# Performance work log

Measured on AMD Instinct MI355X. Metric: run time of the kernel, lower is better.

Reference implementation:

```python
import jax, jax.numpy as jnp
import numpy as np

D = 1024
BATCH = 32768
QJL_DIM = 1024

# Optimal 3-bit (8-level) Lloyd-Max quantizer for the standard normal N(0,1).
# Rotated coordinates of Gaussian inputs are ~N(0,1) since Pi is orthogonal.
_CENTROIDS = np.array([-2.1520, -1.3439, -0.7560, -0.2451,
                        0.2451,  0.7560,  1.3439,  2.1520], dtype=np.float32)
_BOUNDARIES = np.array([-1.7480, -1.0500, -0.5006, 0.0,
                         0.5006,  1.0500,  1.7480], dtype=np.float32)


def setup_inputs() -> dict:
    key = jax.random.key(0)
    kx, kpi, ks = jax.random.split(key, 3)
    x = jax.random.normal(kx, (BATCH, D), dtype=jnp.float32)
    # Haar rotation: orthogonal matrix via QR of a Gaussian matrix
    G = jax.random.normal(kpi, (D, D), dtype=jnp.float32)
    Pi, _ = jnp.linalg.qr(G)
    # QJL projection matrix: iid N(0,1), shape (m, d)
    S = jax.random.normal(ks, (QJL_DIM, D), dtype=jnp.float32)
    return {
        "x": x,
        "Pi": Pi,
        "S": S,
        "centroids": jnp.asarray(_CENTROIDS),
        "boundaries": jnp.asarray(_BOUNDARIES),
    }


def reference(x, Pi, S, centroids, boundaries):
    # --- Stage 1: MSE quantizer (rotate -> Lloyd-Max -> unrotate) ---
    y = x @ Pi.T                                  # (B, d) rotated coordinates
    idx = jnp.searchsorted(boundaries, y)         # (B, d) int32 in [0, 8)
    y_hat = centroids[idx]                        # (B, d) per-coordinate dequant
    x_hat = y_hat @ Pi                            # unrotate back to original frame

    # --- Stage 2: QJL on the residual ---
    residual = x - x_hat                          # (B, d)
    residual_norm = jnp.linalg.norm(residual, axis=-1)   # (B,)
    projected = residual @ S.T                    # (B, m)
    # torch.sign with sign(0) forced to +1
    qjl_signs = jnp.where(projected >= 0, 1.0, -1.0).astype(x.dtype)

    return (idx, qjl_signs, residual_norm)
```

## Files before the change

### kernel.cpp

```cpp
#include <hip/hip_runtime.h>

#define DK 1024
#define NB 32768
#define BM 128
#define BN 128
#define BKT 32
#define NKT (DK / BKT)
#define FLUSH_KT 15

typedef const __attribute__((address_space(1))) void GAS;
typedef __attribute__((address_space(3))) void LAS;

__device__ __forceinline__ void gll16(const void* g, void* l) {
    __builtin_amdgcn_global_load_lds((GAS*)g, (LAS*)l, 16, 0, 0);
}

template<int MODE>
__global__ __launch_bounds__(256)
void gk(const float* __restrict__ A,
        const float* __restrict__ W,
        const float* __restrict__ X,
        const float* __restrict__ cent,
        const float* __restrict__ bnd,
        float* __restrict__ out)
{
    __shared__ float As[2][BM * BKT];
    __shared__ float Bs[2][BN * BKT];
    __shared__ float centS[8];

    const int tid  = threadIdx.x;
    const int lane = tid & 63;
    const int wid  = tid >> 6;
    const int tx8 = tid & 15, ty8 = tid >> 4;
    const int m0 = blockIdx.y * BM;
    const int n0 = blockIdx.x * BN;

    const int lr = lane >> 3;
    const int gs = lane & 7;

    const int arow = tid >> 1;
    const int ah   = (tid & 1) * 4;
    const int akey = (arow >> 3) & 7;
    float4 pidx[4];

    if (MODE == 1 && tid < 8) centS[tid] = cent[tid];

    auto stageNT = [&](float* dst, const float* src, int rowbase, int kt) {
#pragma unroll
        for (int q = 0; q < 4; ++q) {
            const int rb  = wid * 32 + q * 8;
            const int key = (rb >> 3) & 7;
            const float* gp = src + (size_t)(rowbase + rb + lr) * DK
                                  + kt * BKT + ((gs ^ key) << 2);
            gll16(gp, dst + rb * BKT);
        }
    };
    auto stageNN = [&](float* dst, const float* src, int kt) {
#pragma unroll
        for (int q = 0; q < 4; ++q) {
            const int r2 = (wid * 4 + q) * 2;
            const float* gp = src + (size_t)(kt * BKT + r2 + (lane >> 5)) * DK
                                  + n0 + ((lane & 31) << 2);
            gll16(gp, dst + r2 * BN);
        }
    };
    auto loadIdx = [&](int kt) {
#pragma unroll
        for (int g = 0; g < 4; ++g)
            pidx[g] = *(const float4*)&A[(size_t)(m0 + arow) * DK + kt * BKT + (ah + g) * 4];
    };
    auto writeA = [&](float* dst) {
#pragma unroll
        for (int g = 0; g < 4; ++g) {
            float4 v;
            v.x = centS[(int)pidx[g].x];
            v.y = centS[(int)pidx[g].y];
            v.z = centS[(int)pidx[g].z];
            v.w = centS[(int)pidx[g].w];
            *(float4*)&dst[arow * BKT + (((ah + g) ^ akey) << 2)] = v;
        }
    };

    float chn[8][8];
#pragma unroll
    for (int i = 0; i < 8; ++i)
#pragma unroll
        for (int j = 0; j < 8; ++j) chn[i][j] = 0.0f;

    const int akr = ty8 & 7;
    const int bkr = tx8 & 7;

    if (MODE == 1) { loadIdx(0); stageNN(Bs[0], W, 0); }
    else           { stageNT(As[0], A, m0, 0); stageNT(Bs[0], W, n0, 0); }
    __syncthreads();
    if (MODE == 1) { writeA(As[0]); __syncthreads(); }

    int cur = 0;
    for (int kt = 0; kt < NKT; ++kt) {
        if (kt + 1 < NKT) {
            if (MODE == 1) { loadIdx(kt + 1); stageNN(Bs[cur ^ 1], W, kt + 1); }
            else { stageNT(As[cur ^ 1], A, m0, kt + 1);
                   stageNT(Bs[cur ^ 1], W, n0, kt + 1); }
        }

        const float4* As4 = (const float4*)As[cur];
        const float4* Bs4 = (const float4*)Bs[cur];
#pragma unroll
        for (int c = 0; c < 8; ++c) {
            float4 a4[8];
#pragma unroll
            for (int i = 0; i < 8; ++i)
                a4[i] = As4[(ty8 * 8 + i) * 8 + (c ^ akr)];
            if constexpr (MODE != 1) {
                float4 b4[8];
#pragma unroll
                for (int j = 0; j < 8; ++j)
                    b4[j] = Bs4[(tx8 * 8 + j) * 8 + (c ^ bkr)];
#pragma unroll
                for (int e = 0; e < 4; ++e)
#pragma unroll
                    for (int i = 0; i < 8; ++i)
#pragma unroll
                        for (int j = 0; j < 8; ++j)
                            chn[i][j] = fmaf(((const float*)&a4[i])[e],
                                             ((const float*)&b4[j])[e], chn[i][j]);
            } else {
#pragma unroll
                for (int e = 0; e < 4; ++e) {
                    const float4 b0 = *(const float4*)&Bs[cur][(c * 4 + e) * BN + tx8 * 8];
                    const float4 b1 = *(const float4*)&Bs[cur][(c * 4 + e) * BN + tx8 * 8 + 4];
                    const float b[8] = {b0.x, b0.y, b0.z, b0.w, b1.x, b1.y, b1.z, b1.w};
#pragma unroll
                    for (int i = 0; i < 8; ++i)
#pragma unroll
                        for (int j = 0; j < 8; ++j)
                            chn[i][j] = fmaf(((const float*)&a4[i])[e], b[j], chn[i][j]);
                }
            }
        }

        if (kt == FLUSH_KT) {
#pragma unroll
            for (int i = 0; i < 8; ++i) {
                const int row = m0 + ty8 * 8 + i;
#pragma unroll
                for (int jq = 0; jq < 2; ++jq) {
                    float4 v;
                    v.x = chn[i][jq * 4 + 0];
                    v.y = chn[i][jq * 4 + 1];
                    v.z = chn[i][jq * 4 + 2];
                    v.w = chn[i][jq * 4 + 3];
                    *(float4*)&out[(size_t)row * DK + n0 + tx8 * 8 + jq * 4] = v;
                    chn[i][jq * 4 + 0] = 0.0f;
                    chn[i][jq * 4 + 1] = 0.0f;
                    chn[i][jq * 4 + 2] = 0.0f;
                    chn[i][jq * 4 + 3] = 0.0f;
                }
            }
        }

        if (MODE == 1 && kt + 1 < NKT) writeA(As[cur ^ 1]);
        __syncthreads();
        cur ^= 1;
    }

    if constexpr (MODE == 0) {
        float bb[7];
#pragma unroll
        for (int t = 0; t < 7; ++t) bb[t] = bnd[t];
#pragma unroll
        for (int i = 0; i < 8; ++i) {
            const int row = m0 + ty8 * 8 + i;
#pragma unroll
            for (int jq = 0; jq < 2; ++jq) {
                const int col = n0 + tx8 * 8 + jq * 4;
                const float4 p = *(const float4*)&out[(size_t)row * DK + col];
                float4 v;
#pragma unroll
                for (int e = 0; e < 4; ++e) {
                    const float yf = ((const float*)&p)[e] + chn[i][jq * 4 + e];
                    int id = 0;
#pragma unroll
                    for (int t = 0; t < 7; ++t) id += (yf > bb[t]) ? 1 : 0;
                    ((float*)&v)[e] = (float)id;
                }
                *(float4*)&out[(size_t)row * DK + col] = v;
            }
        }
    } else if constexpr (MODE == 1) {
#pragma unroll
        for (int i = 0; i < 8; ++i) {
            const int row = m0 + ty8 * 8 + i;
#pragma unroll
            for (int jq = 0; jq < 2; ++jq) {
                const int col = n0 + tx8 * 8 + jq * 4;
                const float4 p  = *(const float4*)&out[(size_t)row * DK + col];
                const float4 xv = *(const float4*)&X[(size_t)row * DK + col];
                float4 v;
                v.x = xv.x - (p.x + chn[i][jq * 4 + 0]);
                v.y = xv.y - (p.y + chn[i][jq * 4 + 1]);
                v.z = xv.z - (p.z + chn[i][jq * 4 + 2]);
                v.w = xv.w - (p.w + chn[i][jq * 4 + 3]);
                *(float4*)&out[(size_t)row * DK + col] = v;
            }
        }
    } else {
#pragma unroll
        for (int i = 0; i < 8; ++i) {
            const int row = m0 + ty8 * 8 + i;
#pragma unroll
            for (int jq = 0; jq < 2; ++jq) {
                const int col = n0 + tx8 * 8 + jq * 4;
                const float4 p = *(const float4*)&out[(size_t)row * DK + col];
                float4 v;
#pragma unroll
                for (int e = 0; e < 4; ++e)
                    ((float*)&v)[e] =
                        ((((const float*)&p)[e] + chn[i][jq * 4 + e]) >= 0.0f)
                            ? 1.0f : -1.0f;
                *(float4*)&out[(size_t)row * DK + col] = v;
            }
        }
    }
}

__global__ __launch_bounds__(256)
void norm_k(const float* __restrict__ resid, float* __restrict__ outn)
{
    const int lane = threadIdx.x & 63;
    const int row  = blockIdx.x * 4 + (threadIdx.x >> 6);
    const float* r = &resid[(size_t)row * DK];
    double s = 0.0;
    for (int i = lane; i < DK; i += 64) {
        const double v = (double)r[i];
        s += v * v;
    }
#pragma unroll
    for (int off = 32; off > 0; off >>= 1)
        s += __shfl_xor(s, off, 64);
    if (lane == 0) outn[row] = (float)sqrt(s);
}

__global__ __launch_bounds__(256)
void stage2_band(const float* __restrict__ RS,
                 const float* __restrict__ Sm,
                 float* __restrict__ out_sign,
                 float* __restrict__ out_norm)
{
    __shared__ float Rs[16][DK + 1];
    __shared__ float Bsh[16][64];

    const int tid = threadIdx.x;
    const int m0  = blockIdx.x * 16;

    for (int c = tid; c < 16 * 256; c += 256) {
        const int row = c >> 8, q = c & 255;
        const float4 v = *(const float4*)&RS[(size_t)(m0 + row) * DK + q * 4];
        Rs[row][q * 4 + 0] = v.x;
        Rs[row][q * 4 + 1] = v.y;
        Rs[row][q * 4 + 2] = v.z;
        Rs[row][q * 4 + 3] = v.w;
    }
    __syncthreads();

    {
        const int row = tid >> 4, sub = tid & 15;
        double s = 0.0;
        for (int c = sub; c < DK; c += 16) {
            const double v = (double)Rs[row][c];
            s += v * v;
        }
        s += __shfl_xor(s, 1, 16);
        s += __shfl_xor(s, 2, 16);
        s += __shfl_xor(s, 4, 16);
        s += __shfl_xor(s, 8, 16);
        if (sub == 0) out_norm[m0 + row] = (float)sqrt(s);
    }

    const int tx = tid & 15, ty = tid >> 4;
    const int srow = tid >> 2, s4 = tid & 3;

    for (int nt = 0; nt < 16; ++nt) {
        const int n0 = nt * 64;
        float chn[4] = {0.f, 0.f, 0.f, 0.f}, tot[4] = {0.f, 0.f, 0.f, 0.f};

        for (int kt = 0; kt < 64; ++kt) {
            const int k0 = kt * 16;
            __syncthreads();
            const float4 w = *(const float4*)&Sm[(size_t)(n0 + srow) * DK + k0 + s4 * 4];
            Bsh[s4 * 4 + 0][srow] = w.x;
            Bsh[s4 * 4 + 1][srow] = w.y;
            Bsh[s4 * 4 + 2][srow] = w.z;
            Bsh[s4 * 4 + 3][srow] = w.w;
            __syncthreads();
#pragma unroll
            for (int kk = 0; kk < 16; ++kk) {
                const float a = Rs[ty][k0 + kk];
#pragma unroll
                for (int j = 0; j < 4; ++j)
                    chn[j] = fmaf(a, Bsh[kk][tx * 4 + j], chn[j]);
            }
            if (kt == 31) {
#pragma unroll
                for (int j = 0; j < 4; ++j) { tot[j] += chn[j]; chn[j] = 0.0f; }
            }
        }
#pragma unroll
        for (int j = 0; j < 4; ++j) tot[j] += chn[j];
#pragma unroll
        for (int j = 0; j < 4; ++j)
            out_sign[(size_t)(m0 + ty) * DK + n0 + tx * 4 + j] =
                (tot[j] >= 0.0f) ? 1.0f : -1.0f;
    }
}

extern "C" void kernel_launch(void* const* d_in, const int* in_sizes, int n_in,
                              void* d_out, int out_size, void* d_ws, size_t ws_size,
                              hipStream_t stream)
{
    const float* x    = (const float*)d_in[0];
    const float* Pi   = (const float*)d_in[1];
    const float* S    = (const float*)d_in[2];
    const float* cent = (const float*)d_in[3];
    const float* bnd  = (const float*)d_in[4];

    float* out_idx  = (float*)d_out;
    float* out_sign = out_idx + (size_t)NB * DK;
    float* out_norm = out_idx + 2 * (size_t)NB * DK;

    const dim3 grid(DK / BN, NB / BM);
    const size_t needF32 = (size_t)NB * DK * sizeof(float);

    gk<0><<<grid, 256, 0, stream>>>(x, Pi, (const float*)nullptr, cent, bnd, out_idx);

    if (ws_size >= needF32) {
        float* resid = (float*)d_ws;
        gk<1><<<grid, 256, 0, stream>>>(out_idx, Pi, x, cent, bnd, resid);
        gk<2><<<grid, 256, 0, stream>>>(resid, S, (const float*)nullptr, cent, bnd, out_sign);
        norm_k<<<NB / 4, 256, 0, stream>>>(resid, out_norm);
    } else {
        gk<1><<<grid, 256, 0, stream>>>(out_idx, Pi, x, cent, bnd, out_sign);
        stage2_band<<<NB / 16, 256, 0, stream>>>(out_sign, S, out_sign, out_norm);
    }
}
```

Measured before the change: 3.383 ms.

## Read A operand directly from global and emit dequantized y_hat from stage one

After: 3.292 ms. 1.03x faster.

```diff
diff --git a/kernel.cpp b/kernel.cpp
--- a/kernel.cpp
+++ b/kernel.cpp
@@ -22,9 +22,9 @@
         const float* __restrict__ X,
         const float* __restrict__ cent,
         const float* __restrict__ bnd,
-        float* __restrict__ out)
+        float* __restrict__ out,
+        float* __restrict__ yout)
 {
-    __shared__ float As[2][BM * BKT];
     __shared__ float Bs[2][BN * BKT];
     __shared__ float centS[8];
 
@@ -38,19 +38,14 @@
     const int lr = lane >> 3;
     const int gs = lane & 7;
 
-    const int arow = tid >> 1;
-    const int ah   = (tid & 1) * 4;
-    const int akey = (arow >> 3) & 7;
-    float4 pidx[4];
-
-    if (MODE == 1 && tid < 8) centS[tid] = cent[tid];
-
-    auto stageNT = [&](float* dst, const float* src, int rowbase, int kt) {
+    if (MODE == 0 && tid < 8) centS[tid] = cent[tid];
+
+    auto stageNT = [&](float* dst, const float* src, int kt) {
 #pragma unroll
         for (int q = 0; q < 4; ++q) {
             const int rb  = wid * 32 + q * 8;
             const int key = (rb >> 3) & 7;
-            const float* gp = src + (size_t)(rowbase + rb + lr) * DK
+            const float* gp = src + (size_t)(n0 + rb + lr) * DK
                                   + kt * BKT + ((gs ^ key) << 2);
             gll16(gp, dst + rb * BKT);
         }
@@ -64,22 +59,9 @@
             gll16(gp, dst + r2 * BN);
         }
     };
-    auto loadIdx = [&](int kt) {
-#pragma unroll
-        for (int g = 0; g < 4; ++g)
-            pidx[g] = *(const float4*)&A[(size_t)(m0 + arow) * DK + kt * BKT + (ah + g) * 4];
-    };
-    auto writeA = [&](float* dst) {
-#pragma unroll
-        for (int g = 0; g < 4; ++g) {
-            float4 v;
-            v.x = centS[(int)pidx[g].x];
-            v.y = centS[(int)pidx[g].y];
-            v.z = centS[(int)pidx[g].z];
-            v.w = centS[(int)pidx[g].w];
-            *(float4*)&dst[arow * BKT + (((ah + g) ^ akey) << 2)] = v;
-        }
-    };
+
+    const float* aRow = A + (size_t)(m0 + ty8 * 8) * DK;
+    const int bkr = tx8 & 7;
 
     float chn[8][8];
 #pragma unroll
@@ -87,43 +69,41 @@
 #pragma unroll
         for (int j = 0; j < 8; ++j) chn[i][j] = 0.0f;
 
-    const int akr = ty8 & 7;
-    const int bkr = tx8 & 7;
-
-    if (MODE == 1) { loadIdx(0); stageNN(Bs[0], W, 0); }
-    else           { stageNT(As[0], A, m0, 0); stageNT(Bs[0], W, n0, 0); }
+    if (MODE == 1) stageNN(Bs[0], W, 0); else stageNT(Bs[0], W, 0);
     __syncthreads();
-    if (MODE == 1) { writeA(As[0]); __syncthreads(); }
 
     int cur = 0;
     for (int kt = 0; kt < NKT; ++kt) {
         if (kt + 1 < NKT) {
-            if (MODE == 1) { loadIdx(kt + 1); stageNN(Bs[cur ^ 1], W, kt + 1); }
-            else { stageNT(As[cur ^ 1], A, m0, kt + 1);
-                   stageNT(Bs[cur ^ 1], W, n0, kt + 1); }
-        }
-
-        const float4* As4 = (const float4*)As[cur];
+            if (MODE == 1) stageNN(Bs[cur ^ 1], W, kt + 1);
+            else           stageNT(Bs[cur ^ 1], W, kt + 1);
+        }
+
         const float4* Bs4 = (const float4*)Bs[cur];
 #pragma unroll
         for (int c = 0; c < 8; ++c) {
             float4 a4[8];
 #pragma unroll
             for (int i = 0; i < 8; ++i)
-                a4[i] = As4[(ty8 * 8 + i) * 8 + (c ^ akr)];
+                a4[i] = *(const float4*)(aRow + (size_t)i * DK + kt * BKT + c * 4);
+
             if constexpr (MODE != 1) {
-                float4 b4[8];
-#pragma unroll
-                for (int j = 0; j < 8; ++j)
-                    b4[j] = Bs4[(tx8 * 8 + j) * 8 + (c ^ bkr)];
-#pragma unroll
-                for (int e = 0; e < 4; ++e)
-#pragma unroll
-                    for (int i = 0; i < 8; ++i)
-#pragma unroll
-                        for (int j = 0; j < 8; ++j)
-                            chn[i][j] = fmaf(((const float*)&a4[i])[e],
-                                             ((const float*)&b4[j])[e], chn[i][j]);
+#pragma unroll
+                for (int jh = 0; jh < 4; ++jh) {
+                    const float4 b0 = Bs4[(tx8 * 8 + jh * 2) * 8 + (c ^ bkr)];
+                    const float4 b1 = Bs4[(tx8 * 8 + jh * 2 + 1) * 8 + (c ^ bkr)];
+#pragma unroll
+                    for (int e = 0; e < 4; ++e) {
+                        const float be0 = ((const float*)&b0)[e];
+                        const float be1 = ((const float*)&b1)[e];
+#pragma unroll
+                        for (int i = 0; i < 8; ++i) {
+                            const float ae = ((const float*)&a4[i])[e];
+                            chn[i][jh * 2]     = fmaf(ae, be0, chn[i][jh * 2]);
+                            chn[i][jh * 2 + 1] = fmaf(ae, be1, chn[i][jh * 2 + 1]);
+                        }
+                    }
+                }
             } else {
 #pragma unroll
                 for (int e = 0; e < 4; ++e) {
@@ -131,10 +111,12 @@
                     const float4 b1 = *(const float4*)&Bs[cur][(c * 4 + e) * BN + tx8 * 8 + 4];
                     const float b[8] = {b0.x, b0.y, b0.z, b0.w, b1.x, b1.y, b1.z, b1.w};
 #pragma unroll
-                    for (int i = 0; i < 8; ++i)
+                    for (int i = 0; i < 8; ++i) {
+                        const float ae = ((const float*)&a4[i])[e];
 #pragma unroll
                         for (int j = 0; j < 8; ++j)
-                            chn[i][j] = fmaf(((const float*)&a4[i])[e], b[j], chn[i][j]);
+                            chn[i][j] = fmaf(ae, b[j], chn[i][j]);
+                    }
                 }
             }
         }
@@ -159,7 +141,6 @@
             }
         }
 
-        if (MODE == 1 && kt + 1 < NKT) writeA(As[cur ^ 1]);
         __syncthreads();
         cur ^= 1;
     }
@@ -175,16 +156,18 @@
             for (int jq = 0; jq < 2; ++jq) {
                 const int col = n0 + tx8 * 8 + jq * 4;
                 const float4 p = *(const float4*)&out[(size_t)row * DK + col];
-                float4 v;
+                float4 v, yv;
 #pragma unroll
                 for (int e = 0; e < 4; ++e) {
                     const float yf = ((const float*)&p)[e] + chn[i][jq * 4 + e];
                     int id = 0;
 #pragma unroll
                     for (int t = 0; t < 7; ++t) id += (yf > bb[t]) ? 1 : 0;
-                    ((float*)&v)[e] = (float)id;
-                }
-                *(float4*)&out[(size_t)row * DK + col] = v;
+                    ((float*)&v)[e]  = (float)id;
+                    ((float*)&yv)[e] = centS[id];
+                }
+                *(float4*)&out[(size_t)row * DK + col]  = v;
+                *(float4*)&yout[(size_t)row * DK + col] = yv;
             }
         }
     } else if constexpr (MODE == 1) {
@@ -225,6 +208,138 @@
 }
 
 __global__ __launch_bounds__(256)
+void gk1_lut(const float* __restrict__ IDXF,
+             const float* __restrict__ W,
+             const float* __restrict__ X,
+             const float* __restrict__ cent,
+             float* __restrict__ out)
+{
+    __shared__ float As[2][BM * BKT];
+    __shared__ float Bs[2][BN * BKT];
+    __shared__ float centS[8];
+
+    const int tid  = threadIdx.x;
+    const int lane = tid & 63;
+    const int wid  = tid >> 6;
+    const int tx8 = tid & 15, ty8 = tid >> 4;
+    const int m0 = blockIdx.y * BM;
+    const int n0 = blockIdx.x * BN;
+
+    const int arow = tid >> 1;
+    const int ah   = (tid & 1) * 4;
+    const int akey = (arow >> 3) & 7;
+    float4 pidx[4];
+
+    if (tid < 8) centS[tid] = cent[tid];
+
+    auto stageNN = [&](float* dst, const float* src, int kt) {
+#pragma unroll
+        for (int q = 0; q < 4; ++q) {
+            const int r2 = (wid * 4 + q) * 2;
+            const float* gp = src + (size_t)(kt * BKT + r2 + (lane >> 5)) * DK
+                                  + n0 + ((lane & 31) << 2);
+            gll16(gp, dst + r2 * BN);
+        }
+    };
+    auto loadIdx = [&](int kt) {
+#pragma unroll
+        for (int g = 0; g < 4; ++g)
+            pidx[g] = *(const float4*)&IDXF[(size_t)(m0 + arow) * DK + kt * BKT + (ah + g) * 4];
+    };
+    auto writeA = [&](float* dst) {
+#pragma unroll
+        for (int g = 0; g < 4; ++g) {
+            float4 v;
+            v.x = centS[(int)pidx[g].x];
+            v.y = centS[(int)pidx[g].y];
+            v.z = centS[(int)pidx[g].z];
+            v.w = centS[(int)pidx[g].w];
+            *(float4*)&dst[arow * BKT + (((ah + g) ^ akey) << 2)] = v;
+        }
+    };
+
+    float chn[8][8];
+#pragma unroll
+    for (int i = 0; i < 8; ++i)
+#pragma unroll
+        for (int j = 0; j < 8; ++j) chn[i][j] = 0.0f;
+
+    const int akr = ty8 & 7;
+
+    loadIdx(0); stageNN(Bs[0], W, 0);
+    __syncthreads();
+    writeA(As[0]); __syncthreads();
+
+    int cur = 0;
+    for (int kt = 0; kt < NKT; ++kt) {
+        if (kt + 1 < NKT) { loadIdx(kt + 1); stageNN(Bs[cur ^ 1], W, kt + 1); }
+
+        const float4* As4 = (const float4*)As[cur];
+#pragma unroll
+        for (int c = 0; c < 8; ++c) {
+            float4 a4[8];
+#pragma unroll
+            for (int i = 0; i < 8; ++i)
+                a4[i] = As4[(ty8 * 8 + i) * 8 + (c ^ akr)];
+#pragma unroll
+            for (int e = 0; e < 4; ++e) {
+                const float4 b0 = *(const float4*)&Bs[cur][(c * 4 + e) * BN + tx8 * 8];
+                const float4 b1 = *(const float4*)&Bs[cur][(c * 4 + e) * BN + tx8 * 8 + 4];
+                const float b[8] = {b0.x, b0.y, b0.z, b0.w, b1.x, b1.y, b1.z, b1.w};
+#pragma unroll
+                for (int i = 0; i < 8; ++i) {
+                    const float ae = ((const float*)&a4[i])[e];
+#pragma unroll
+                    for (int j = 0; j < 8; ++j)
+                        chn[i][j] = fmaf(ae, b[j], chn[i][j]);
+                }
+            }
+        }
+
+        if (kt == FLUSH_KT) {
+#pragma unroll
+            for (int i = 0; i < 8; ++i) {
+                const int row = m0 + ty8 * 8 + i;
+#pragma unroll
+                for (int jq = 0; jq < 2; ++jq) {
+                    float4 v;
+                    v.x = chn[i][jq * 4 + 0];
+                    v.y = chn[i][jq * 4 + 1];
+                    v.z = chn[i][jq * 4 + 2];
+                    v.w = chn[i][jq * 4 + 3];
+                    *(float4*)&out[(size_t)row * DK + n0 + tx8 * 8 + jq * 4] = v;
+                    chn[i][jq * 4 + 0] = 0.0f;
+                    chn[i][jq * 4 + 1] = 0.0f;
+                    chn[i][jq * 4 + 2] = 0.0f;
+                    chn[i][jq * 4 + 3] = 0.0f;
+                }
+            }
+        }
+
+        if (kt + 1 < NKT) writeA(As[cur ^ 1]);
+        __syncthreads();
+        cur ^= 1;
+    }
+
+#pragma unroll
+    for (int i = 0; i < 8; ++i) {
+        const int row = m0 + ty8 * 8 + i;
+#pragma unroll
+        for (int jq = 0; jq < 2; ++jq) {
+            const int col = n0 + tx8 * 8 + jq * 4;
+            const float4 p  = *(const float4*)&out[(size_t)row * DK + col];
+            const float4 xv = *(const float4*)&X[(size_t)row * DK + col];
+            float4 v;
+            v.x = xv.x - (p.x + chn[i][jq * 4 + 0]);
+            v.y = xv.y - (p.y + chn[i][jq * 4 + 1]);
+            v.z = xv.z - (p.z + chn[i][jq * 4 + 2]);
+            v.w = xv.w - (p.w + chn[i][jq * 4 + 3]);
+            *(float4*)&out[(size_t)row * DK + col] = v;
+        }
+    }
+}
+
+__global__ __launch_bounds__(256)
 void norm_k(const float* __restrict__ resid, float* __restrict__ outn)
 {
     const int lane = threadIdx.x & 63;
@@ -331,15 +446,18 @@
     const dim3 grid(DK / BN, NB / BM);
     const size_t needF32 = (size_t)NB * DK * sizeof(float);
 
-    gk<0><<<grid, 256, 0, stream>>>(x, Pi, (const float*)nullptr, cent, bnd, out_idx);
+    gk<0><<<grid, 256, 0, stream>>>(x, Pi, (const float*)nullptr, cent, bnd,
+                                    out_idx, out_sign);
 
     if (ws_size >= needF32) {
         float* resid = (float*)d_ws;
-        gk<1><<<grid, 256, 0, stream>>>(out_idx, Pi, x, cent, bnd, resid);
-        gk<2><<<grid, 256, 0, stream>>>(resid, S, (const float*)nullptr, cent, bnd, out_sign);
+        gk<1><<<grid, 256, 0, stream>>>(out_sign , Pi, x, cent, bnd,
+                                        resid, (float*)nullptr);
+        gk<2><<<grid, 256, 0, stream>>>(resid, S, (const float*)nullptr, cent, bnd,
+                                        out_sign, (float*)nullptr);
         norm_k<<<NB / 4, 256, 0, stream>>>(resid, out_norm);
     } else {
-        gk<1><<<grid, 256, 0, stream>>>(out_idx, Pi, x, cent, bnd, out_sign);
+        gk1_lut<<<grid, 256, 0, stream>>>(out_idx, Pi, x, cent, out_sign);
         stage2_band<<<NB / 16, 256, 0, stream>>>(out_sign, S, out_sign, out_norm);
     }
 }
```
